# Kernel optimization log

Measured on AMD Instinct MI355X. Metric: run time of the kernel, lower is better.

Reference implementation:

```python
import jax, jax.numpy as jnp
import numpy as np
import math

EPS = 1e-6
TEMPERATURE = 1.0
NEG = -100.0


def setup_inputs() -> dict:
    key = jax.random.key(0)
    k1, k2, k3 = jax.random.split(key, 3)
    B, N, C = 16, 2048, 64
    x = jax.random.normal(k1, (B, N, C), dtype=jnp.float32)
    y = jax.random.normal(k2, (B, N, C), dtype=jnp.float32)
    # complementary keep / pruned gates, as produced by the TPS token scorer
    keep = jax.random.bernoulli(k3, 0.5, (B, N, 1)).astype(jnp.float32)
    pruned = 1.0 - keep
    return {
        "x": x,
        "y": y,
        "current_keep_decision": keep,
        "current_pruned_decision": pruned,
    }


def reference(x, y, current_keep_decision, current_pruned_decision):
    # Training branch of TPSModule.forward (module defaults to training mode).
    B, N, C = x.shape
    # --- get_sim(x, None, mask_eye=-100, l2_norm=True) ---
    xn = x / (jnp.linalg.norm(x, axis=-1, keepdims=True) + EPS)
    sim = jnp.einsum("bnc,bmc->bnm", xn, xn)  # [B, N, N]
    eye = jnp.eye(N, dtype=bool)
    sim = jnp.where(eye[None, :, :], NEG, sim)
    sim = sim / TEMPERATURE
    # mask out columns of non-kept tokens
    keep_b = current_keep_decision.reshape(B, 1, N).astype(bool)
    sim = jnp.where(keep_b, sim, NEG)
    # hard top-1 (with ties) per row, gated by pruned flag of the source row
    sim_th = jnp.max(sim, axis=2, keepdims=True)  # [B, N, 1]
    mask = (sim == sim_th).astype(x.dtype) * current_pruned_decision  # [B, N, N]
    cos = mask * sim
    # transpose: now rows index destination (kept) tokens
    mask_t = mask.transpose(0, 2, 1)
    cos_t = cos.transpose(0, 2, 1)
    numerator = jnp.exp(cos_t) * mask_t  # [B, N, N]
    denominator = math.e + jnp.sum(numerator, axis=-1, keepdims=True)  # [B, N, 1]
    out = x * (math.e / denominator) + jnp.einsum(
        "bnm,bmc->bnc", numerator / denominator, x
    )
    return out
```

## Files before the change

kernel.cpp:

```cpp
#include <hip/hip_runtime.h>
#include <math.h>

#define BB 16
#define NN 2048
#define CC 64
#define TPB 256
#define MROWS 16
#define RPW 4
#define E_CONST 2.71828182845904523536f

__global__ __launch_bounds__(TPB) void k_pre(const float* __restrict__ keep,
                                             float* __restrict__ outz,
                                             float* __restrict__ S,
                                             int* __restrict__ cntP,
                                             int* __restrict__ cntK,
                                             int* __restrict__ listP,
                                             int* __restrict__ listK) {
    const int tid = threadIdx.x, lane = tid & 63;

    float4* o4 = (float4*)outz + (size_t)blockIdx.x * 1024;
    float4 z = {0.0f, 0.0f, 0.0f, 0.0f};
#pragma unroll
    for (int i = 0; i < 4; ++i) o4[i * TPB + tid] = z;

    const int b = blockIdx.x;
    if (b >= BB) return;

    __shared__ int cP, cK;
    if (tid == 0) { cP = 0; cK = 0; }
    __syncthreads();
    for (int i = tid; i < NN; i += TPB) S[b * NN + i] = 0.0f;
    const unsigned long long lt = (lane == 63) ? 0x7fffffffffffffffull
                                               : ((1ull << lane) - 1ull);
#pragma unroll
    for (int it = 0; it < NN / TPB; ++it) {
        int n = it * TPB + tid;
        bool kp = keep[b * NN + n] != 0.0f;
        unsigned long long mk = __ballot(kp);
        int nk = __popcll(mk);
        int bk = 0, bp = 0;
        if (lane == 0) {
            bk = atomicAdd(&cK, nk);
            bp = atomicAdd(&cP, 64 - nk);
        }
        bk = __shfl(bk, 0); bp = __shfl(bp, 0);
        int pk = __popcll(mk & lt);
        if (kp) listK[b * NN + bk + pk] = n;
        else    listP[b * NN + bp + (lane - pk)] = n;
    }
    __syncthreads();
    if (tid == 0) { cntP[b] = cP; cntK[b] = cK; }
}

__global__ __launch_bounds__(TPB) void k_pre2(const float* __restrict__ x,
                                              const int* __restrict__ cntK,
                                              const int* __restrict__ listK,
                                              float4* __restrict__ colM) {
    const int b = blockIdx.y;
    const int colp = blockIdx.x * TPB + threadIdx.x;
    const int K = cntK[b];
    bool ok = colp < K;
    int tok = ok ? listK[b * NN + colp] : 0;
    const float4* x4 = (const float4*)(x + (size_t)b * NN * CC);
    float4 v[16];
    float sq = 0.0f;
#pragma unroll
    for (int k4 = 0; k4 < 16; ++k4) {
        v[k4] = x4[(size_t)tok * 16 + k4];
        sq += v[k4].x * v[k4].x + v[k4].y * v[k4].y
            + v[k4].z * v[k4].z + v[k4].w * v[k4].w;
    }
    float iv = ok ? 1.0f / (sqrtf(sq) + 1e-6f) : 0.0f;
#pragma unroll
    for (int k4 = 0; k4 < 16; ++k4) {
        float4 w = v[k4];
        w.x *= iv; w.y *= iv; w.z *= iv; w.w *= iv;
        colM[((size_t)b * 16 + k4) * NN + colp] = w;
    }
}

__global__ __launch_bounds__(TPB, 4) void k_argmax(
    const float* __restrict__ x,
    const float4* __restrict__ colM,
    const int*   __restrict__ cntP,
    const int*   __restrict__ cntK,
    const int*   __restrict__ listP,
    const int*   __restrict__ listK,
    float* __restrict__ S,
    float* __restrict__ A) {

    const int b    = blockIdx.x & 15;
    const int tile = blockIdx.x >> 4;
    const int P = cntP[b], K = cntK[b];
    const int base = tile * MROWS;
    if (base >= P) return;

    const int tid = threadIdx.x;
    const int wid = tid >> 6;
    const int lane = tid & 63;

    int rtok[RPW];
#pragma unroll
    for (int r = 0; r < RPW; ++r) {
        int rid = base + wid * RPW + r;
        int tok = (rid < P) ? listP[b * NN + rid] : 0;
        rtok[r] = __builtin_amdgcn_readfirstlane(tok);
    }
    const float4* x4 = (const float4*)(x + (size_t)b * NN * CC);
    const float4* cm = colM + (size_t)b * 16 * NN;

    float    tmax[RPW];
    unsigned msk[RPW];
#pragma unroll
    for (int r = 0; r < RPW; ++r) { tmax[r] = -3.0e38f; msk[r] = 0u; }

    const int ntiles = (K + 511) >> 9;

    for (int t = 0; t < ntiles; ++t) {
        const int cstart = t * 512;

        float acc[RPW][8];
#pragma unroll
        for (int r = 0; r < RPW; ++r)
#pragma unroll
            for (int j = 0; j < 8; ++j) acc[r][j] = 0.0f;

#pragma unroll 2
        for (int k4 = 0; k4 < 16; ++k4) {
            float4 rv[RPW];
#pragma unroll
            for (int r = 0; r < RPW; ++r)
                rv[r] = x4[(size_t)rtok[r] * 16 + k4];
            const float4* cmk = cm + (size_t)k4 * NN + cstart + lane;
            float4 cv[8];
#pragma unroll
            for (int j = 0; j < 8; ++j)
                cv[j] = cmk[j * 64];
#pragma unroll
            for (int r = 0; r < RPW; ++r)
#pragma unroll
                for (int j = 0; j < 8; ++j)
                    acc[r][j] = fmaf(rv[r].x, cv[j].x,
                                fmaf(rv[r].y, cv[j].y,
                                fmaf(rv[r].z, cv[j].z,
                                fmaf(rv[r].w, cv[j].w, acc[r][j]))));
        }

#pragma unroll
        for (int r = 0; r < RPW; ++r)
#pragma unroll
            for (int j = 0; j < 8; ++j) {
                int colp = cstart + j * 64 + lane;
                float s = (colp < K) ? acc[r][j] : -1.0e30f;
                unsigned bit = 1u << ((t << 3) | j);
                if (s > tmax[r])       { tmax[r] = s; msk[r] = bit; }
                else if (s == tmax[r])  msk[r] |= bit;
            }
    }

    int nvr = P - base - wid * RPW;
    for (int r = 0; r < RPW; ++r) {
        if (r >= nvr) break;
        float m = tmax[r];
#pragma unroll
        for (int off = 32; off; off >>= 1) m = fmaxf(m, __shfl_xor(m, off, 64));
        int src = rtok[r];
        float xv = x[(size_t)(b * NN + src) * CC + lane];
        float sq = xv * xv;
#pragma unroll
        for (int off = 32; off; off >>= 1) sq += __shfl_xor(sq, off, 64);
        float ivr = 1.0f / (sqrtf(sq) + 1e-6f);
        float wgt = expf(m * ivr);
        unsigned long long bal = __ballot(tmax[r] == m && msk[r] != 0u);
        while (bal) {
            int sl = __ffsll(bal) - 1;
            bal &= bal - 1;
            unsigned mm = __shfl(msk[r], sl);
            while (mm) {
                int bit = __ffs(mm) - 1;
                mm &= mm - 1;
                int colp = ((bit >> 3) * 512) + ((bit & 7) * 64) + sl;
                int dst = listK[b * NN + colp];
                atomicAdd(&A[(size_t)(b * NN + dst) * CC + lane], wgt * xv);
                if (lane == 0) atomicAdd(&S[b * NN + dst], wgt);
            }
        }
    }
}

__global__ __launch_bounds__(TPB) void k_finalize(const float* __restrict__ x,
                                                  const float* __restrict__ S,
                                                  float* __restrict__ out) {
    int i = blockIdx.x * TPB + threadIdx.x;
    int row = i >> 4;
    float inv = 1.0f / (E_CONST + S[row]);
    float4 xv = ((const float4*)x)[i];
    float4 av = ((float4*)out)[i];
    float4 o;
    o.x = (xv.x * E_CONST + av.x) * inv;
    o.y = (xv.y * E_CONST + av.y) * inv;
    o.z = (xv.z * E_CONST + av.z) * inv;
    o.w = (xv.w * E_CONST + av.w) * inv;
    ((float4*)out)[i] = o;
}

extern "C" void kernel_launch(void* const* d_in, const int* in_sizes, int n_in,
                              void* d_out, int out_size, void* d_ws, size_t ws_size,
                              hipStream_t stream) {
    const float* x    = (const float*)d_in[0];
    const float* keep = (const float*)d_in[2];
    float* out = (float*)d_out;

    char* ws = (char*)d_ws;
    float* S    = (float*)(ws + (128 << 10));
    int*   cntP = (int*)(ws + (256 << 10));
    int*   cntK = cntP + 16;
    int*   listP = (int*)(ws + (256 << 10) + 128);
    int*   listK = listP + BB * NN;
    float4* colM = (float4*)(ws + (1 << 20));

    k_pre<<<512, TPB, 0, stream>>>(keep, out, S, cntP, cntK, listP, listK);

    dim3 gp2(NN / TPB, BB);
    k_pre2<<<gp2, TPB, 0, stream>>>(x, cntK, listK, colM);

    k_argmax<<<(NN / MROWS) * BB, TPB, 0, stream>>>(x, colM, cntP, cntK,
                                                    listP, listK, S, out);

    k_finalize<<<(BB * NN * CC / 4) / TPB, TPB, 0, stream>>>(x, S, out);
}
```

Before: 147.5 us.

## Split argmax columns across waves so each block loads column tiles once

In the similarity argmax kernel, each wave now takes all 16 source rows of the block and a 128-column slice of every 512-column tile. Before, each wave took 4 rows and swept every column. This removes the fourfold redundant loading of the normalized column matrix across the block's waves. Row vectors, which are wave-uniform, are now read by every wave instead. The per-row maximum is combined across waves through shared memory with a block barrier, and the tie bitmask encoding is adjusted to the new column mapping.

```diff
diff --git a/kernel.cpp b/kernel.cpp
--- a/kernel.cpp
+++ b/kernel.cpp
@@ -6,7 +6,6 @@
 #define CC 64
 #define TPB 256
 #define MROWS 16
-#define RPW 4
 #define E_CONST 2.71828182845904523536f
 
 __global__ __launch_bounds__(TPB) void k_pre(const float* __restrict__ keep,
@@ -99,71 +98,74 @@
     const int wid = tid >> 6;
     const int lane = tid & 63;
 
-    int rtok[RPW];
-#pragma unroll
-    for (int r = 0; r < RPW; ++r) {
-        int rid = base + wid * RPW + r;
+    __shared__ float wm[4][MROWS];
+
+    int rtok[MROWS];
+#pragma unroll
+    for (int r = 0; r < MROWS; ++r) {
+        int rid = base + r;
         int tok = (rid < P) ? listP[b * NN + rid] : 0;
         rtok[r] = __builtin_amdgcn_readfirstlane(tok);
     }
     const float4* x4 = (const float4*)(x + (size_t)b * NN * CC);
     const float4* cm = colM + (size_t)b * 16 * NN;
 
-    float    tmax[RPW];
-    unsigned msk[RPW];
-#pragma unroll
-    for (int r = 0; r < RPW; ++r) { tmax[r] = -3.0e38f; msk[r] = 0u; }
+    float    tmax[MROWS];
+    unsigned msk[MROWS];
+#pragma unroll
+    for (int r = 0; r < MROWS; ++r) { tmax[r] = -3.0e38f; msk[r] = 0u; }
 
     const int ntiles = (K + 511) >> 9;
 
     for (int t = 0; t < ntiles; ++t) {
-        const int cstart = t * 512;
-
-        float acc[RPW][8];
-#pragma unroll
-        for (int r = 0; r < RPW; ++r)
-#pragma unroll
-            for (int j = 0; j < 8; ++j) acc[r][j] = 0.0f;
-
-#pragma unroll 2
+        const int cstart = t * 512 + wid * 128;
+        if (cstart >= K) break;
+
+        float acc[MROWS][2];
+#pragma unroll
+        for (int r = 0; r < MROWS; ++r) { acc[r][0] = 0.0f; acc[r][1] = 0.0f; }
+
+#pragma unroll 4
         for (int k4 = 0; k4 < 16; ++k4) {
-            float4 rv[RPW];
-#pragma unroll
-            for (int r = 0; r < RPW; ++r)
-                rv[r] = x4[(size_t)rtok[r] * 16 + k4];
-            const float4* cmk = cm + (size_t)k4 * NN + cstart + lane;
-            float4 cv[8];
-#pragma unroll
-            for (int j = 0; j < 8; ++j)
-                cv[j] = cmk[j * 64];
-#pragma unroll
-            for (int r = 0; r < RPW; ++r)
-#pragma unroll
-                for (int j = 0; j < 8; ++j)
-                    acc[r][j] = fmaf(rv[r].x, cv[j].x,
-                                fmaf(rv[r].y, cv[j].y,
-                                fmaf(rv[r].z, cv[j].z,
-                                fmaf(rv[r].w, cv[j].w, acc[r][j]))));
+            const float4* cb = cm + (size_t)k4 * NN + cstart + lane;
+            float4 cv0 = cb[0];
+            float4 cv1 = cb[64];
+#pragma unroll
+            for (int r = 0; r < MROWS; ++r) {
+                float4 rv = x4[(size_t)rtok[r] * 16 + k4];
+                acc[r][0] = fmaf(rv.x, cv0.x, fmaf(rv.y, cv0.y,
+                            fmaf(rv.z, cv0.z, fmaf(rv.w, cv0.w, acc[r][0]))));
+                acc[r][1] = fmaf(rv.x, cv1.x, fmaf(rv.y, cv1.y,
+                            fmaf(rv.z, cv1.z, fmaf(rv.w, cv1.w, acc[r][1]))));
+            }
         }
 
 #pragma unroll
-        for (int r = 0; r < RPW; ++r)
-#pragma unroll
-            for (int j = 0; j < 8; ++j) {
+        for (int r = 0; r < MROWS; ++r)
+#pragma unroll
+            for (int j = 0; j < 2; ++j) {
                 int colp = cstart + j * 64 + lane;
                 float s = (colp < K) ? acc[r][j] : -1.0e30f;
-                unsigned bit = 1u << ((t << 3) | j);
+                unsigned bit = 1u << ((t << 1) | j);
                 if (s > tmax[r])       { tmax[r] = s; msk[r] = bit; }
                 else if (s == tmax[r])  msk[r] |= bit;
             }
     }
 
-    int nvr = P - base - wid * RPW;
-    for (int r = 0; r < RPW; ++r) {
+#pragma unroll
+    for (int r = 0; r < MROWS; ++r) {
+        float m = tmax[r];
+#pragma unroll
+        for (int off = 32; off; off >>= 1) m = fmaxf(m, __shfl_xor(m, off, 64));
+        if (lane == 0) wm[wid][r] = m;
+    }
+    __syncthreads();
+
+    const int nvr = min(MROWS, P - base);
+#pragma unroll
+    for (int r = 0; r < MROWS; ++r) {
         if (r >= nvr) break;
-        float m = tmax[r];
-#pragma unroll
-        for (int off = 32; off; off >>= 1) m = fmaxf(m, __shfl_xor(m, off, 64));
+        float m = fmaxf(fmaxf(wm[0][r], wm[1][r]), fmaxf(wm[2][r], wm[3][r]));
         int src = rtok[r];
         float xv = x[(size_t)(b * NN + src) * CC + lane];
         float sq = xv * xv;
@@ -179,7 +181,7 @@
             while (mm) {
                 int bit = __ffs(mm) - 1;
                 mm &= mm - 1;
-                int colp = ((bit >> 3) * 512) + ((bit & 7) * 64) + sl;
+                int colp = (bit >> 1) * 512 + wid * 128 + (bit & 1) * 64 + sl;
                 int dst = listK[b * NN + colp];
                 atomicAdd(&A[(size_t)(b * NN + dst) * CC + lane], wgt * xv);
                 if (lane == 0) atomicAdd(&S[b * NN + dst], wgt);
```

New measurement: 237.6 us. 61.1% more time.
